# Kernel optimization log

Hardware: AMD Instinct MI355X
Metric: run time of the kernel (lower is better)

## Reference

```python
import jax, jax.numpy as jnp
import numpy as np

B, CIN, COUT, H, W = 4, 256, 256, 64, 64
K, G = 3, 4
PAD = (K - 1) // 2


def setup_inputs() -> dict:
    key = jax.random.key(0)
    k0, k1, k2, k3 = jax.random.split(key, 4)
    x = jax.random.normal(k0, (B, CIN, H, W), jnp.float32)
    y = jax.random.normal(k1, (B, 2, H, W), jnp.float32)
    # conv_offset: 1x1 conv, no bias, init std=0.1 (normal_init)
    w_offset = jax.random.normal(k2, (G * 2 * K * K, 2, 1, 1), jnp.float32) * 0.1
    # DeformConv2d weight, no bias, init std=0.01
    w_deform = jax.random.normal(k3, (COUT, CIN, K, K), jnp.float32) * 0.01
    return {"x": x, "y": y, "w_offset": w_offset, "w_deform": w_deform}


def _deform_conv(x, offset, weight):
    """DCN v1: stride 1, dilation 1, zero padding PAD, deform_groups=G, groups=1."""
    KK = K * K
    # mmcv offset layout: [B, G*2*KK, H, W] -> per group, per kernel pos, (dy, dx)
    off = offset.reshape(B, G, KK, 2, H, W)
    dy, dx = off[:, :, :, 0], off[:, :, :, 1]            # [B,G,KK,H,W]
    ii, jj = jnp.meshgrid(jnp.arange(K), jnp.arange(K), indexing="ij")
    ky = ii.reshape(KK).astype(x.dtype)                  # kernel row offsets
    kx = jj.reshape(KK).astype(x.dtype)                  # kernel col offsets
    base_y = jnp.arange(H, dtype=x.dtype)[None, :, None] - PAD + ky[:, None, None]  # [KK,H,1]
    base_x = jnp.arange(W, dtype=x.dtype)[None, None, :] - PAD + kx[:, None, None]  # [KK,1,W]
    yc = dy + base_y                                     # [B,G,KK,H,W]
    xc = dx + base_x

    Cg = CIN // G
    xg = x.reshape(B, G, Cg, H, W)

    def sample(xg1, yc1, xc1):
        # xg1 [Cg,H,W]; yc1/xc1 [KK,H,W] -> bilinear sample with zero padding
        y0 = jnp.floor(yc1)
        x0 = jnp.floor(xc1)
        wy = yc1 - y0
        wx = xc1 - x0
        y0i = y0.astype(jnp.int32)
        x0i = x0.astype(jnp.int32)

        def gather(yi, xi):
            valid = (yi >= 0) & (yi < H) & (xi >= 0) & (xi < W)
            v = xg1[:, jnp.clip(yi, 0, H - 1), jnp.clip(xi, 0, W - 1)]  # [Cg,KK,H,W]
            return v * valid[None].astype(xg1.dtype)

        v00 = gather(y0i, x0i)
        v01 = gather(y0i, x0i + 1)
        v10 = gather(y0i + 1, x0i)
        v11 = gather(y0i + 1, x0i + 1)
        return (v00 * (1 - wy) * (1 - wx) + v01 * (1 - wy) * wx
                + v10 * wy * (1 - wx) + v11 * wy * wx)

    sampled = jax.vmap(jax.vmap(sample))(xg, yc, xc)     # [B,G,Cg,KK,H,W]
    sampled = sampled.reshape(B, CIN, KK, H, W)
    wflat = weight.reshape(COUT, CIN, KK)
    return jnp.einsum("bckhw,ock->bohw", sampled, wflat)  # [B,COUT,H,W]


def reference(x, y, w_offset, w_deform):
    # offset = conv_offset(y.detach()), a 1x1 conv without bias
    y_det = jax.lax.stop_gradient(y)
    offset = jnp.einsum("bihw,oi->bohw", y_det, w_offset[:, :, 0, 0])
    out = _deform_conv(x, offset, w_deform)
    return jax.nn.relu(out)
```

## Files before the change

### kernel.cpp

```cpp
#include <hip/hip_runtime.h>
#include <cstddef>

#define B_    4
#define CIN_  256
#define COUT_ 256
#define H_    64
#define W_    64
#define KK_   9
#define G_    4
#define PAD_  1
#define TPX   64
#define NSL   18

typedef short bf16x8 __attribute__((ext_vector_type(8)));
typedef float f32x4  __attribute__((ext_vector_type(4)));
typedef __attribute__((address_space(1))) const unsigned int* gptr_t;
typedef __attribute__((address_space(3))) unsigned int*       lptr_t;

__device__ __forceinline__ unsigned short f2bf(float v) {
    unsigned int u = __float_as_uint(v);
    u += 0x7fffu + ((u >> 16) & 1u);
    return (unsigned short)(u >> 16);
}
__device__ __forceinline__ float f_lo(unsigned int u) { return __uint_as_float(u << 16); }
__device__ __forceinline__ float f_hi(unsigned int u) { return __uint_as_float(u & 0xffff0000u); }

__global__ __launch_bounds__(256) void xt_kernel(const float* __restrict__ x,
                                                 unsigned short* __restrict__ xT) {
    __shared__ unsigned short s[128][66];
    const int tid   = threadIdx.x;
    const int bh    = blockIdx.x >> 1;
    const int chalf = blockIdx.x & 1;
    const size_t src_base = ((size_t)(bh >> 6) * CIN_ + chalf * 128) * (H_ * W_) + (bh & 63) * W_;
    #pragma unroll 4
    for (int k = 0; k < 32; ++k) {
        int i = k * 256 + tid;
        int c = i >> 6, w = i & 63;
        s[c][w] = f2bf(x[src_base + (size_t)c * (H_ * W_) + w]);
    }
    __syncthreads();
    #pragma unroll 4
    for (int k = 0; k < 16; ++k) {
        int j  = k * 256 + tid;
        int c2 = (j & 63) * 2, w = j >> 6;
        unsigned int lo = s[c2][w], hi = s[c2 + 1][w];
        *(unsigned int*)(xT + ((size_t)bh * 64 + w) * 256 + chalf * 128 + c2) = lo | (hi << 16);
    }
}

__global__ __launch_bounds__(256) void wt_kernel(const float* __restrict__ w,
                                                 unsigned short* __restrict__ wb) {
    int idx = blockIdx.x * 256 + threadIdx.x;
    int e   = idx & 7;
    int pos = (idx >> 3) & 7;
    int o   = (idx >> 6) & 255;
    int t   = idx >> 14;
    int g   = t / 9, kk = t - g * 9;
    int j   = pos ^ (o & 7);
    int c   = g * 64 + j * 8 + e;
    wb[idx] = f2bf(w[(o * CIN_ + c) * KK_ + kk]);
}

__global__ __launch_bounds__(512, 4) void dcn_kernel(
    const unsigned short* __restrict__ xT, const float* __restrict__ y,
    const float* __restrict__ w_off, const unsigned short* __restrict__ wb,
    float* __restrict__ part0, float* __restrict__ part1)
{
    __shared__ unsigned short s_W[COUT_ * 64];
    __shared__ unsigned short s_S[TPX * 64];

    const int tid = threadIdx.x;
    const int bid   = blockIdx.x;
    const int xcd   = bid & 7;
    const int b     = xcd >> 1;
    const int khalf = xcd & 1;
    const int h     = bid >> 3;

    const int sp = tid & 63;
    const int c8 = tid >> 6;

    const float yv0 = y[((b * 2 + 0) * H_ + h) * W_ + sp];
    const float yv1 = y[((b * 2 + 1) * H_ + h) * W_ + sp];

    const int lane = tid & 63, wave = tid >> 6;
    const int pg  = wave & 1, oh = wave >> 1;
    const int l15 = lane & 15, kq = lane >> 4, sw = l15 & 7;

    f32x4 acc[8];
    #pragma unroll
    for (int i = 0; i < 8; ++i) acc[i] = (f32x4){0.f, 0.f, 0.f, 0.f};

    const size_t xbase = (size_t)b * (H_ * W_ * 256) + c8 * 8;

    for (int sl = 0; sl < NSL; ++sl) {
        const int s  = khalf * NSL + sl;
        const int g  = khalf * 2 + sl / 9;
        const int kk = sl % 9;

        __syncthreads();

        {
            const unsigned short* src = wb + (size_t)s * 16384;
            #pragma unroll
            for (int j = 0; j < 4; ++j) {
                const int off = (j * 512 + tid) * 8;
                __builtin_amdgcn_global_load_lds((gptr_t)(src + off),
                                                 (lptr_t)(s_W + off), 16, 0, 0);
            }
        }

        {
            const float4 co = *(const float4*)(w_off + s * 4);
            const float dy = fmaf(yv0, co.x, yv1 * co.y);
            const float dx = fmaf(yv0, co.z, yv1 * co.w);
            const float yc = (float)(h + (kk / 3) - PAD_) + dy;
            const float xc = (float)(sp + (kk % 3) - PAD_) + dx;
            const float yf = floorf(yc), xf = floorf(xc);
            const float wy = yc - yf,    wx = xc - xf;
            const int   yi = (int)yf,    xi = (int)xf;
            float w00 = (1.f - wy) * (1.f - wx);
            float w01 = (1.f - wy) * wx;
            float w10 = wy * (1.f - wx);
            float w11 = wy * wx;
            const bool y0ok = (yi >= 0) & (yi < H_);
            const bool y1ok = (yi >= -1) & (yi < H_ - 1);
            const bool x0ok = (xi >= 0) & (xi < W_);
            const bool x1ok = (xi >= -1) & (xi < W_ - 1);
            w00 = (y0ok & x0ok) ? w00 : 0.f;
            w01 = (y0ok & x1ok) ? w01 : 0.f;
            w10 = (y1ok & x0ok) ? w10 : 0.f;
            w11 = (y1ok & x1ok) ? w11 : 0.f;
            const int y0c = min(max(yi, 0), H_ - 1);
            const int y1c = min(max(yi + 1, 0), H_ - 1);
            const int x0c = min(max(xi, 0), W_ - 1);
            const int x1c = min(max(xi + 1, 0), W_ - 1);
            const unsigned short* xb = xT + xbase + g * 64;
            const uint4 A  = *(const uint4*)(xb + ((size_t)y0c * W_ + x0c) * 256);
            const uint4 Bv = *(const uint4*)(xb + ((size_t)y0c * W_ + x1c) * 256);
            const uint4 C  = *(const uint4*)(xb + ((size_t)y1c * W_ + x0c) * 256);
            const uint4 D  = *(const uint4*)(xb + ((size_t)y1c * W_ + x1c) * 256);
            const unsigned int av[4] = {A.x, A.y, A.z, A.w};
            const unsigned int bv[4] = {Bv.x, Bv.y, Bv.z, Bv.w};
            const unsigned int cv[4] = {C.x, C.y, C.z, C.w};
            const unsigned int dv[4] = {D.x, D.y, D.z, D.w};
            unsigned int res[4];
            #pragma unroll
            for (int q = 0; q < 4; ++q) {
                float rl = w00 * f_lo(av[q]);
                rl = fmaf(w01, f_lo(bv[q]), rl);
                rl = fmaf(w10, f_lo(cv[q]), rl);
                rl = fmaf(w11, f_lo(dv[q]), rl);
                float rh = w00 * f_hi(av[q]);
                rh = fmaf(w01, f_hi(bv[q]), rh);
                rh = fmaf(w10, f_hi(cv[q]), rh);
                rh = fmaf(w11, f_hi(dv[q]), rh);
                res[q] = __builtin_amdgcn_perm(__float_as_uint(rh),
                                               __float_as_uint(rl), 0x07060302u);
            }
            *(uint4*)(s_S + sp * 64 + ((c8 ^ (sp & 7)) * 8)) =
                make_uint4(res[0], res[1], res[2], res[3]);
        }

        __syncthreads();

        bf16x8 bf[2][2], af[2][4];
        #pragma unroll
        for (int kh = 0; kh < 2; ++kh) {
            const int pos = ((kh * 4 + kq) ^ sw) * 8;
            #pragma unroll
            for (int nt = 0; nt < 2; ++nt)
                bf[kh][nt] = *(const bf16x8*)(s_S + (pg * 32 + nt * 16 + l15) * 64 + pos);
            #pragma unroll
            for (int mt = 0; mt < 4; ++mt)
                af[kh][mt] = *(const bf16x8*)(s_W + (oh * 64 + mt * 16 + l15) * 64 + pos);
        }
        #pragma unroll
        for (int kh = 0; kh < 2; ++kh)
            #pragma unroll
            for (int nt = 0; nt < 2; ++nt)
                #pragma unroll
                for (int mt = 0; mt < 4; ++mt)
                    acc[nt * 4 + mt] = __builtin_amdgcn_mfma_f32_16x16x32_bf16(
                        af[kh][mt], bf[kh][nt], acc[nt * 4 + mt], 0, 0, 0);
    }

    float* dst = khalf ? part1 : part0;
    #pragma unroll
    for (int nt = 0; nt < 2; ++nt) {
        const int px = pg * 32 + nt * 16 + l15;
        #pragma unroll
        for (int mt = 0; mt < 4; ++mt) {
            const int obase = oh * 64 + mt * 16 + kq * 4;
            #pragma unroll
            for (int r = 0; r < 4; ++r) {
                dst[(((size_t)b * COUT_ + obase + r) * H_ + h) * W_ + px] =
                    acc[nt * 4 + mt][r];
            }
        }
    }
}

__global__ __launch_bounds__(256) void red_kernel(const float4* __restrict__ p1,
                                                  float4* __restrict__ out) {
    const int i = blockIdx.x * 256 + threadIdx.x;
    float4 a = out[i];
    float4 b = p1[i];
    float4 r;
    r.x = fmaxf(a.x + b.x, 0.f);
    r.y = fmaxf(a.y + b.y, 0.f);
    r.z = fmaxf(a.z + b.z, 0.f);
    r.w = fmaxf(a.w + b.w, 0.f);
    out[i] = r;
}

extern "C" void kernel_launch(void* const* d_in, const int* in_sizes, int n_in,
                              void* d_out, int out_size, void* d_ws, size_t ws_size,
                              hipStream_t stream) {
    const float* x     = (const float*)d_in[0];
    const float* y     = (const float*)d_in[1];
    const float* w_off = (const float*)d_in[2];
    const float* w_def = (const float*)d_in[3];
    float* out = (float*)d_out;

    unsigned short* xT = (unsigned short*)d_ws;
    unsigned short* wb = (unsigned short*)d_ws + 4194304;
    float* part1 = (float*)((char*)d_ws + 9568256);

    xt_kernel<<<B_ * H_ * 2, 256, 0, stream>>>(x, xT);
    wt_kernel<<<(36 * 16384) / 256, 256, 0, stream>>>(w_def, wb);
    dcn_kernel<<<512, 512, 0, stream>>>(xT, y, w_off, wb, out, part1);
    red_kernel<<<(B_ * COUT_ * H_ * W_) / 4 / 256, 256, 0, stream>>>(
        (const float4*)part1, (float4*)out);
}
```

Before: 134.0 us.

## Fuse prep kernels, drop K-split, double-buffer DCN sampling and weight staging

```diff
diff --git a/kernel.cpp b/kernel.cpp
--- a/kernel.cpp
+++ b/kernel.cpp
@@ -9,8 +9,7 @@
 #define KK_   9
 #define G_    4
 #define PAD_  1
-#define TPX   64
-#define NSL   18
+#define NSL   36
 
 typedef short bf16x8 __attribute__((ext_vector_type(8)));
 typedef float f32x4  __attribute__((ext_vector_type(4)));
@@ -25,59 +24,59 @@
 __device__ __forceinline__ float f_lo(unsigned int u) { return __uint_as_float(u << 16); }
 __device__ __forceinline__ float f_hi(unsigned int u) { return __uint_as_float(u & 0xffff0000u); }
 
-__global__ __launch_bounds__(256) void xt_kernel(const float* __restrict__ x,
-                                                 unsigned short* __restrict__ xT) {
-    __shared__ unsigned short s[128][66];
-    const int tid   = threadIdx.x;
-    const int bh    = blockIdx.x >> 1;
-    const int chalf = blockIdx.x & 1;
-    const size_t src_base = ((size_t)(bh >> 6) * CIN_ + chalf * 128) * (H_ * W_) + (bh & 63) * W_;
-    #pragma unroll 4
-    for (int k = 0; k < 32; ++k) {
-        int i = k * 256 + tid;
-        int c = i >> 6, w = i & 63;
-        s[c][w] = f2bf(x[src_base + (size_t)c * (H_ * W_) + w]);
+__global__ __launch_bounds__(256) void prep_kernel(const float* __restrict__ x,
+                                                   unsigned short* __restrict__ xT,
+                                                   const float* __restrict__ w,
+                                                   unsigned short* __restrict__ wb) {
+    const int tid = threadIdx.x;
+    if (blockIdx.x < 512) {
+        __shared__ unsigned short s[128][66];
+        const int bh    = blockIdx.x >> 1;
+        const int chalf = blockIdx.x & 1;
+        const size_t src_base = ((size_t)(bh >> 6) * CIN_ + chalf * 128) * (H_ * W_) + (bh & 63) * W_;
+        #pragma unroll 4
+        for (int k = 0; k < 32; ++k) {
+            int i = k * 256 + tid;
+            int c = i >> 6, ww = i & 63;
+            s[c][ww] = f2bf(x[src_base + (size_t)c * (H_ * W_) + ww]);
+        }
+        __syncthreads();
+        #pragma unroll 4
+        for (int k = 0; k < 16; ++k) {
+            int j  = k * 256 + tid;
+            int c2 = (j & 63) * 2, ww = j >> 6;
+            unsigned int lo = s[c2][ww], hi = s[c2 + 1][ww];
+            *(unsigned int*)(xT + ((size_t)bh * 64 + ww) * 256 + chalf * 128 + c2) = lo | (hi << 16);
+        }
+    } else {
+        int idx = (blockIdx.x - 512) * 256 + tid;
+        int e   = idx & 7;
+        int pos = (idx >> 3) & 7;
+        int o   = (idx >> 6) & 255;
+        int t   = idx >> 14;
+        int g   = t / 9, kk = t - g * 9;
+        int j   = pos ^ (o & 7);
+        int c   = g * 64 + j * 8 + e;
+        wb[idx] = f2bf(w[(o * CIN_ + c) * KK_ + kk]);
     }
-    __syncthreads();
-    #pragma unroll 4
-    for (int k = 0; k < 16; ++k) {
-        int j  = k * 256 + tid;
-        int c2 = (j & 63) * 2, w = j >> 6;
-        unsigned int lo = s[c2][w], hi = s[c2 + 1][w];
-        *(unsigned int*)(xT + ((size_t)bh * 64 + w) * 256 + chalf * 128 + c2) = lo | (hi << 16);
-    }
-}
-
-__global__ __launch_bounds__(256) void wt_kernel(const float* __restrict__ w,
-                                                 unsigned short* __restrict__ wb) {
-    int idx = blockIdx.x * 256 + threadIdx.x;
-    int e   = idx & 7;
-    int pos = (idx >> 3) & 7;
-    int o   = (idx >> 6) & 255;
-    int t   = idx >> 14;
-    int g   = t / 9, kk = t - g * 9;
-    int j   = pos ^ (o & 7);
-    int c   = g * 64 + j * 8 + e;
-    wb[idx] = f2bf(w[(o * CIN_ + c) * KK_ + kk]);
-}
-
-__global__ __launch_bounds__(512, 4) void dcn_kernel(
+}
+
+__global__ __launch_bounds__(512, 2) void dcn_kernel(
     const unsigned short* __restrict__ xT, const float* __restrict__ y,
     const float* __restrict__ w_off, const unsigned short* __restrict__ wb,
-    float* __restrict__ part0, float* __restrict__ part1)
+    float* __restrict__ out)
 {
-    __shared__ unsigned short s_W[COUT_ * 64];
-    __shared__ unsigned short s_S[TPX * 64];
+    __shared__ unsigned short s_W[2][COUT_ * 64];
+    __shared__ unsigned short s_S[2][64 * 64];
 
     const int tid = threadIdx.x;
-    const int bid   = blockIdx.x;
-    const int xcd   = bid & 7;
-    const int b     = xcd >> 1;
-    const int khalf = xcd & 1;
-    const int h     = bid >> 3;
-
-    const int sp = tid & 63;
-    const int c8 = tid >> 6;
+    const int bid = blockIdx.x;
+    const int xcd = bid & 7;
+    const int b   = xcd >> 1;
+    const int h   = (xcd & 1) * 32 + (bid >> 3);
+
+    const int sp = tid >> 3;
+    const int c8 = tid & 7;
 
     const float yv0 = y[((b * 2 + 0) * H_ + h) * W_ + sp];
     const float yv1 = y[((b * 2 + 1) * H_ + h) * W_ + sp];
@@ -92,99 +91,124 @@
 
     const size_t xbase = (size_t)b * (H_ * W_ * 256) + c8 * 8;
 
-    for (int sl = 0; sl < NSL; ++sl) {
-        const int s  = khalf * NSL + sl;
-        const int g  = khalf * 2 + sl / 9;
-        const int kk = sl % 9;
-
+    float w00, w01, w10, w11;
+    uint4 A, Bv, C, D;
+
+#define ISSUE_SAMPLE(t) do {                                                   \
+    const int g_ = (t) / 9, kk_ = (t) % 9;                                     \
+    const float4 co = *(const float4*)(w_off + (t) * 4);                       \
+    const float dy = fmaf(yv0, co.x, yv1 * co.y);                              \
+    const float dx = fmaf(yv0, co.z, yv1 * co.w);                              \
+    const float yc = (float)(h + (kk_ / 3) - PAD_) + dy;                       \
+    const float xc = (float)(sp + (kk_ % 3) - PAD_) + dx;                      \
+    const float yf = floorf(yc), xf = floorf(xc);                              \
+    const float wy = yc - yf,    wx = xc - xf;                                 \
+    const int   yi = (int)yf,    xi = (int)xf;                                 \
+    float a00 = (1.f - wy) * (1.f - wx);                                       \
+    float a01 = (1.f - wy) * wx;                                               \
+    float a10 = wy * (1.f - wx);                                               \
+    float a11 = wy * wx;                                                       \
+    const bool y0ok = (yi >= 0) & (yi < H_);                                   \
+    const bool y1ok = (yi >= -1) & (yi < H_ - 1);                              \
+    const bool x0ok = (xi >= 0) & (xi < W_);                                   \
+    const bool x1ok = (xi >= -1) & (xi < W_ - 1);                              \
+    w00 = (y0ok & x0ok) ? a00 : 0.f;                                           \
+    w01 = (y0ok & x1ok) ? a01 : 0.f;                                           \
+    w10 = (y1ok & x0ok) ? a10 : 0.f;                                           \
+    w11 = (y1ok & x1ok) ? a11 : 0.f;                                           \
+    const int y0c = min(max(yi, 0), H_ - 1);                                   \
+    const int y1c = min(max(yi + 1, 0), H_ - 1);                               \
+    const int x0c = min(max(xi, 0), W_ - 1);                                   \
+    const int x1c = min(max(xi + 1, 0), W_ - 1);                               \
+    const unsigned short* xb = xT + xbase + g_ * 64;                           \
+    A  = *(const uint4*)(xb + ((size_t)y0c * W_ + x0c) * 256);                 \
+    Bv = *(const uint4*)(xb + ((size_t)y0c * W_ + x1c) * 256);                 \
+    C  = *(const uint4*)(xb + ((size_t)y1c * W_ + x0c) * 256);                 \
+    D  = *(const uint4*)(xb + ((size_t)y1c * W_ + x1c) * 256);                 \
+} while (0)
+
+#define STAGE_W(t, buf) do {                                                   \
+    const unsigned short* src = wb + (size_t)(t) * 16384;                      \
+    _Pragma("unroll")                                                          \
+    for (int j = 0; j < 4; ++j) {                                              \
+        const int off = (j * 512 + tid) * 8;                                   \
+        __builtin_amdgcn_global_load_lds((gptr_t)(src + off),                  \
+                                         (lptr_t)(s_W[buf] + off), 16, 0, 0);  \
+    }                                                                          \
+} while (0)
+
+#define WRITE_SAMPLE(buf) do {                                                 \
+    const unsigned int av[4] = {A.x, A.y, A.z, A.w};                           \
+    const unsigned int bv[4] = {Bv.x, Bv.y, Bv.z, Bv.w};                       \
+    const unsigned int cv[4] = {C.x, C.y, C.z, C.w};                           \
+    const unsigned int dv[4] = {D.x, D.y, D.z, D.w};                           \
+    unsigned int res[4];                                                       \
+    _Pragma("unroll")                                                          \
+    for (int q = 0; q < 4; ++q) {                                              \
+        float rl = w00 * f_lo(av[q]);                                          \
+        rl = fmaf(w01, f_lo(bv[q]), rl);                                       \
+        rl = fmaf(w10, f_lo(cv[q]), rl);                                       \
+        rl = fmaf(w11, f_lo(dv[q]), rl);                                       \
+        float rh = w00 * f_hi(av[q]);                                          \
+        rh = fmaf(w01, f_hi(bv[q]), rh);                                       \
+        rh = fmaf(w10, f_hi(cv[q]), rh);                                       \
+        rh = fmaf(w11, f_hi(dv[q]), rh);                                       \
+        res[q] = __builtin_amdgcn_perm(__float_as_uint(rh),                    \
+                                       __float_as_uint(rl), 0x07060302u);      \
+    }                                                                          \
+    *(uint4*)(s_S[buf] + sp * 64 + ((c8 ^ (sp & 7)) * 8)) =                    \
+        make_uint4(res[0], res[1], res[2], res[3]);                            \
+} while (0)
+
+#define MFMA_STEP(buf) do {                                                    \
+    bf16x8 bf[2][2], af[2][4];                                                 \
+    _Pragma("unroll")                                                          \
+    for (int kh = 0; kh < 2; ++kh) {                                           \
+        const int pos = ((kh * 4 + kq) ^ sw) * 8;                              \
+        _Pragma("unroll")                                                      \
+        for (int nt = 0; nt < 2; ++nt)                                         \
+            bf[kh][nt] = *(const bf16x8*)(s_S[buf] +                           \
+                              (pg * 32 + nt * 16 + l15) * 64 + pos);           \
+        _Pragma("unroll")                                                      \
+        for (int mt = 0; mt < 4; ++mt)                                         \
+            af[kh][mt] = *(const bf16x8*)(s_W[buf] +                           \
+                              (oh * 64 + mt * 16 + l15) * 64 + pos);           \
+    }                                                                          \
+    __builtin_amdgcn_s_setprio(1);                                             \
+    _Pragma("unroll")                                                          \
+    for (int kh = 0; kh < 2; ++kh)                                             \
+        _Pragma("unroll")                                                      \
+        for (int nt = 0; nt < 2; ++nt)                                         \
+            _Pragma("unroll")                                                  \
+            for (int mt = 0; mt < 4; ++mt)                                     \
+                acc[nt * 4 + mt] = __builtin_amdgcn_mfma_f32_16x16x32_bf16(    \
+                    af[kh][mt], bf[kh][nt], acc[nt * 4 + mt], 0, 0, 0);        \
+    __builtin_amdgcn_s_setprio(0);                                             \
+} while (0)
+
+    ISSUE_SAMPLE(0);
+    STAGE_W(0, 0);
+    WRITE_SAMPLE(0);
+    __syncthreads();
+
+    for (int s = 0; s < NSL; s += 2) {
+        ISSUE_SAMPLE(s + 1);
+        STAGE_W(s + 1, 1);
+        __builtin_amdgcn_sched_barrier(0);
+        MFMA_STEP(0);
+        WRITE_SAMPLE(1);
         __syncthreads();
 
-        {
-            const unsigned short* src = wb + (size_t)s * 16384;
-            #pragma unroll
-            for (int j = 0; j < 4; ++j) {
-                const int off = (j * 512 + tid) * 8;
-                __builtin_amdgcn_global_load_lds((gptr_t)(src + off),
-                                                 (lptr_t)(s_W + off), 16, 0, 0);
-            }
-        }
-
-        {
-            const float4 co = *(const float4*)(w_off + s * 4);
-            const float dy = fmaf(yv0, co.x, yv1 * co.y);
-            const float dx = fmaf(yv0, co.z, yv1 * co.w);
-            const float yc = (float)(h + (kk / 3) - PAD_) + dy;
-            const float xc = (float)(sp + (kk % 3) - PAD_) + dx;
-            const float yf = floorf(yc), xf = floorf(xc);
-            const float wy = yc - yf,    wx = xc - xf;
-            const int   yi = (int)yf,    xi = (int)xf;
-            float w00 = (1.f - wy) * (1.f - wx);
-            float w01 = (1.f - wy) * wx;
-            float w10 = wy * (1.f - wx);
-            float w11 = wy * wx;
-            const bool y0ok = (yi >= 0) & (yi < H_);
-            const bool y1ok = (yi >= -1) & (yi < H_ - 1);
-            const bool x0ok = (xi >= 0) & (xi < W_);
-            const bool x1ok = (xi >= -1) & (xi < W_ - 1);
-            w00 = (y0ok & x0ok) ? w00 : 0.f;
-            w01 = (y0ok & x1ok) ? w01 : 0.f;
-            w10 = (y1ok & x0ok) ? w10 : 0.f;
-            w11 = (y1ok & x1ok) ? w11 : 0.f;
-            const int y0c = min(max(yi, 0), H_ - 1);
-            const int y1c = min(max(yi + 1, 0), H_ - 1);
-            const int x0c = min(max(xi, 0), W_ - 1);
-            const int x1c = min(max(xi + 1, 0), W_ - 1);
-            const unsigned short* xb = xT + xbase + g * 64;
-            const uint4 A  = *(const uint4*)(xb + ((size_t)y0c * W_ + x0c) * 256);
-            const uint4 Bv = *(const uint4*)(xb + ((size_t)y0c * W_ + x1c) * 256);
-            const uint4 C  = *(const uint4*)(xb + ((size_t)y1c * W_ + x0c) * 256);
-            const uint4 D  = *(const uint4*)(xb + ((size_t)y1c * W_ + x1c) * 256);
-            const unsigned int av[4] = {A.x, A.y, A.z, A.w};
-            const unsigned int bv[4] = {Bv.x, Bv.y, Bv.z, Bv.w};
-            const unsigned int cv[4] = {C.x, C.y, C.z, C.w};
-            const unsigned int dv[4] = {D.x, D.y, D.z, D.w};
-            unsigned int res[4];
-            #pragma unroll
-            for (int q = 0; q < 4; ++q) {
-                float rl = w00 * f_lo(av[q]);
-                rl = fmaf(w01, f_lo(bv[q]), rl);
-                rl = fmaf(w10, f_lo(cv[q]), rl);
-                rl = fmaf(w11, f_lo(dv[q]), rl);
-                float rh = w00 * f_hi(av[q]);
-                rh = fmaf(w01, f_hi(bv[q]), rh);
-                rh = fmaf(w10, f_hi(cv[q]), rh);
-                rh = fmaf(w11, f_hi(dv[q]), rh);
-                res[q] = __builtin_amdgcn_perm(__float_as_uint(rh),
-                                               __float_as_uint(rl), 0x07060302u);
-            }
-            *(uint4*)(s_S + sp * 64 + ((c8 ^ (sp & 7)) * 8)) =
-                make_uint4(res[0], res[1], res[2], res[3]);
-        }
-
+        if (s + 2 < NSL) {
+            ISSUE_SAMPLE(s + 2);
+            STAGE_W(s + 2, 0);
+        }
+        __builtin_amdgcn_sched_barrier(0);
+        MFMA_STEP(1);
+        if (s + 2 < NSL) WRITE_SAMPLE(0);
         __syncthreads();
-
-        bf16x8 bf[2][2], af[2][4];
-        #pragma unroll
-        for (int kh = 0; kh < 2; ++kh) {
-            const int pos = ((kh * 4 + kq) ^ sw) * 8;
-            #pragma unroll
-            for (int nt = 0; nt < 2; ++nt)
-                bf[kh][nt] = *(const bf16x8*)(s_S + (pg * 32 + nt * 16 + l15) * 64 + pos);
-            #pragma unroll
-            for (int mt = 0; mt < 4; ++mt)
-                af[kh][mt] = *(const bf16x8*)(s_W + (oh * 64 + mt * 16 + l15) * 64 + pos);
-        }
-        #pragma unroll
-        for (int kh = 0; kh < 2; ++kh)
-            #pragma unroll
-            for (int nt = 0; nt < 2; ++nt)
-                #pragma unroll
-                for (int mt = 0; mt < 4; ++mt)
-                    acc[nt * 4 + mt] = __builtin_amdgcn_mfma_f32_16x16x32_bf16(
-                        af[kh][mt], bf[kh][nt], acc[nt * 4 + mt], 0, 0, 0);
     }
 
-    float* dst = khalf ? part1 : part0;
     #pragma unroll
     for (int nt = 0; nt < 2; ++nt) {
         const int px = pg * 32 + nt * 16 + l15;
@@ -193,24 +217,15 @@
             const int obase = oh * 64 + mt * 16 + kq * 4;
             #pragma unroll
             for (int r = 0; r < 4; ++r) {
-                dst[(((size_t)b * COUT_ + obase + r) * H_ + h) * W_ + px] =
-                    acc[nt * 4 + mt][r];
+                out[(((size_t)b * COUT_ + obase + r) * H_ + h) * W_ + px] =
+                    fmaxf(acc[nt * 4 + mt][r], 0.f);
             }
         }
     }
-}
-
-__global__ __launch_bounds__(256) void red_kernel(const float4* __restrict__ p1,
-                                                  float4* __restrict__ out) {
-    const int i = blockIdx.x * 256 + threadIdx.x;
-    float4 a = out[i];
-    float4 b = p1[i];
-    float4 r;
-    r.x = fmaxf(a.x + b.x, 0.f);
-    r.y = fmaxf(a.y + b.y, 0.f);
-    r.z = fmaxf(a.z + b.z, 0.f);
-    r.w = fmaxf(a.w + b.w, 0.f);
-    out[i] = r;
+#undef ISSUE_SAMPLE
+#undef STAGE_W
+#undef WRITE_SAMPLE
+#undef MFMA_STEP
 }
 
 extern "C" void kernel_launch(void* const* d_in, const int* in_sizes, int n_in,
@@ -224,11 +239,7 @@
 
     unsigned short* xT = (unsigned short*)d_ws;
     unsigned short* wb = (unsigned short*)d_ws + 4194304;
-    float* part1 = (float*)((char*)d_ws + 9568256);
-
-    xt_kernel<<<B_ * H_ * 2, 256, 0, stream>>>(x, xT);
-    wt_kernel<<<(36 * 16384) / 256, 256, 0, stream>>>(w_def, wb);
-    dcn_kernel<<<512, 512, 0, stream>>>(xT, y, w_off, wb, out, part1);
-    red_kernel<<<(B_ * COUT_ * H_ * W_) / 4 / 256, 256, 0, stream>>>(
-        (const float4*)part1, (float4*)out);
-}
+
+    prep_kernel<<<2816, 256, 0, stream>>>(x, xT, w_def, wb);
+    dcn_kernel<<<256, 512, 0, stream>>>(xT, y, w_off, wb, out);
+}
```

After: 122.0 us. 9.0% less time.
